# Performance work log

Measured on AMD Instinct MI355X. Metric: run time of the kernel, lower is better.

Reference implementation:

```python
import jax, jax.numpy as jnp
import numpy as np


def setup_inputs() -> dict:
    key = jax.random.key(0)
    ks = jax.random.split(key, 8)
    B, C, H, W = 4, 512, 64, 64
    C8 = C // 8
    return {
        "x": jax.random.normal(ks[0], (B, C, H, W), dtype=jnp.float32),
        "Wq": jax.random.normal(ks[1], (C8, C), dtype=jnp.float32) * 0.02,
        "bq": jax.random.normal(ks[2], (C8,), dtype=jnp.float32) * 0.02,
        "Wk": jax.random.normal(ks[3], (C8, C), dtype=jnp.float32) * 0.02,
        "bk": jax.random.normal(ks[4], (C8,), dtype=jnp.float32) * 0.02,
        "Wv": jax.random.normal(ks[5], (C, C), dtype=jnp.float32) * 0.02,
        "bv": jax.random.normal(ks[6], (C,), dtype=jnp.float32) * 0.02,
        "gamma": jax.random.normal(ks[7], (1,), dtype=jnp.float32),
    }


def reference(x, Wq, bq, Wk, bk, Wv, bv, gamma):
    B, C, H, W = x.shape
    N = H * W
    xf = x.reshape(B, C, N)  # 1x1 conv == per-position matmul over channels
    q = jnp.einsum('oc,bcn->bno', Wq, xf) + bq  # B, N, C//8  (proj_query^T)
    k = jnp.einsum('oc,bcn->bon', Wk, xf) + bk[None, :, None]  # B, C//8, N
    v = jnp.einsum('oc,bcn->bon', Wv, xf) + bv[None, :, None]  # B, C, N
    energy = jnp.einsum('bno,bom->bnm', q, k)  # B, N, N
    attention = jax.nn.softmax(energy, axis=-1)
    # out = bmm(proj_value, attention^T): out[:, :, n] = sum_m v[:, :, m] * att[n, m]
    out = jnp.einsum('bcm,bnm->bcn', v, attention).reshape(B, C, H, W)
    return gamma[0] * out + x
```

## Files before the change

kernel.cpp:

```cpp
#include <hip/hip_runtime.h>
#include <stdint.h>


typedef unsigned short u16;
typedef unsigned char u8;
typedef __attribute__((ext_vector_type(8))) short short8;
typedef __attribute__((ext_vector_type(4))) float f32x4;
typedef __attribute__((ext_vector_type(16))) float f32x16;
typedef __attribute__((ext_vector_type(4))) int i32x4;
typedef __attribute__((ext_vector_type(8))) int i32x8;

#define ASYNC16(gp, lp)                                                        \
  __builtin_amdgcn_global_load_lds(                                            \
      (__attribute__((address_space(1))) void*)(void*)(gp),                    \
      (__attribute__((address_space(3))) void*)(lp), 16, 0, 0)

#define WAIT_VM0 0x0F70
#define WAIT_VM3 0x0F73
#define WAIT_LGKM0 0xC07F

#define EXP_SHIFT 5.0f
#define EXP_CAP 57000.0f

__device__ __forceinline__ u16 f2bf(float f) {
  uint32_t u = __float_as_uint(f);
  u += 0x7FFFu + ((u >> 16) & 1u);
  return (u16)(u >> 16);
}

__device__ __forceinline__ u8 f2fp8(float f) {
  f = fminf(fmaxf(f, -440.f), 440.f);
  int r = __builtin_amdgcn_cvt_pk_fp8_f32(f, f, 0, false);
  return (u8)(r & 0xFF);
}

__global__ __launch_bounds__(256) void k_transpose(const float* __restrict__ x,
                                                   u16* __restrict__ xT) {
  __shared__ float tile[32][33];
  const int b = blockIdx.z;
  const int nb = blockIdx.x * 32;
  const int cb = blockIdx.y * 32;
  const int t = threadIdx.x;
  {
    const int nl = t & 31, c0 = t >> 5;
    const float* xp = x + ((size_t)b * 512 + cb) * 4096 + nb;
#pragma unroll
    for (int i = 0; i < 4; ++i) {
      const int cl = c0 + i * 8;
      tile[cl][nl] = xp[(size_t)cl * 4096 + nl];
    }
  }
  __syncthreads();
  {
    const int cl = t & 31, n0 = t >> 5;
    u16* xtp = xT + ((size_t)b * 4096 + nb) * 512 + cb;
#pragma unroll
    for (int i = 0; i < 4; ++i) {
      const int nl = n0 + i * 8;
      xtp[(size_t)nl * 512 + cl] = f2bf(tile[cl][nl]);
    }
  }
}

__global__ __launch_bounds__(256) void k_wcast(const float* __restrict__ Wq,
                                               const float* __restrict__ Wk,
                                               const float* __restrict__ Wv,
                                               u16* __restrict__ wqk,
                                               u16* __restrict__ wv) {
  const int idx = blockIdx.x * 256 + threadIdx.x;
  if (idx < 128 * 512) {
    const int r = idx >> 9, c = idx & 511;
    const float f = (r < 64) ? Wq[r * 512 + c] : Wk[(r - 64) * 512 + c];
    wqk[idx] = f2bf(f);
  } else {
    const int j = idx - 128 * 512;
    if (j < 512 * 512) wv[j] = f2bf(Wv[j]);
  }
}

__device__ __forceinline__ void gemm_bt_tile(const u16* __restrict__ A,
                                             const u16* __restrict__ B,
                                             const int K, const int rowA0,
                                             const int colB0, u16* smem,
                                             f32x4 acc[4][4]) {
  const int t = threadIdx.x;
  const int lane = t & 63, wave = t >> 6;
  const int quad = lane >> 4, l15 = lane & 15;
  const int wr = wave >> 1, wc = wave & 1;
  u16* As = smem;
  u16* Bs = smem + 8192;
  const f32x4 zero = {0.f, 0.f, 0.f, 0.f};
#pragma unroll
  for (int i = 0; i < 4; ++i)
#pragma unroll
    for (int j = 0; j < 4; ++j) acc[i][j] = zero;

  const int srow = t >> 3;
  const int c8 = (lane & 7) ^ (lane >> 3);
  const u16* ga = A + (size_t)(rowA0 + srow) * K + c8 * 8;
  const u16* gb = B + (size_t)(colB0 + srow) * K + c8 * 8;
  char* la = (char*)As + wave * 1024;
  char* lb = (char*)Bs + wave * 1024;
  const size_t rK32 = (size_t)32 * K;

  const int sw0 = (quad) ^ (l15 & 7);
  const int sw1 = (4 + quad) ^ (l15 & 7);

  for (int k0 = 0; k0 < K; k0 += 64) {
    ASYNC16(ga + k0, la);
    ASYNC16(ga + k0 + rK32, la + 4096);
    ASYNC16(ga + k0 + 2 * rK32, la + 8192);
    ASYNC16(ga + k0 + 3 * rK32, la + 12288);
    ASYNC16(gb + k0, lb);
    ASYNC16(gb + k0 + rK32, lb + 4096);
    ASYNC16(gb + k0 + 2 * rK32, lb + 8192);
    ASYNC16(gb + k0 + 3 * rK32, lb + 12288);
    __syncthreads();
#pragma unroll
    for (int s = 0; s < 2; ++s) {
      const int sw = s ? sw1 : sw0;
      short8 a[4], b[4];
#pragma unroll
      for (int i = 0; i < 4; ++i)
        a[i] = *(const short8*)(As + (wr * 64 + i * 16 + l15) * 64 + sw * 8);
#pragma unroll
      for (int j = 0; j < 4; ++j)
        b[j] = *(const short8*)(Bs + (wc * 64 + j * 16 + l15) * 64 + sw * 8);
#pragma unroll
      for (int i = 0; i < 4; ++i)
#pragma unroll
        for (int j = 0; j < 4; ++j)
          acc[i][j] = __builtin_amdgcn_mfma_f32_16x16x32_bf16(a[i], b[j],
                                                              acc[i][j], 0, 0, 0);
    }
    __syncthreads();
  }
}

__global__ __launch_bounds__(256) void k_proj(const u16* __restrict__ xT,
                                              const u16* __restrict__ wqk,
                                              const u16* __restrict__ wv,
                                              const float* __restrict__ bq,
                                              const float* __restrict__ bk,
                                              const float* __restrict__ bv,
                                              u16* __restrict__ q,
                                              u16* __restrict__ kT,
                                              u8* __restrict__ v8) {
  __shared__ u16 smem[16384];
  const int b = blockIdx.z;
  const int by = blockIdx.y;
  const int t = threadIdx.x, lane = t & 63, wave = t >> 6;
  const int quad = lane >> 4, l15 = lane & 15;
  const int wr = wave >> 1, wc = wave & 1;
  f32x4 acc[4][4];

  if (by == 4) {
    const int rowA0 = blockIdx.x * 128;
    gemm_bt_tile(xT + (size_t)b * 4096 * 512, wqk, 512, rowA0, 0, smem, acc);
#pragma unroll
    for (int j = 0; j < 4; ++j) {
      const int col = wc * 64 + j * 16 + l15;
      const float bias = (col < 64) ? bq[col] : bk[col - 64];
#pragma unroll
      for (int i = 0; i < 4; ++i) {
#pragma unroll
        for (int r = 0; r < 4; ++r) {
          const int row = rowA0 + wr * 64 + i * 16 + quad * 4 + r;
          const float val = acc[i][j][r] + bias;
          if (col < 64)
            q[((size_t)b * 4096 + row) * 64 + col] = f2bf(val);
          else
            kT[((size_t)b * 4096 + row) * 64 + (col - 64)] = f2bf(val);
        }
      }
    }
  } else {
    const int rowA0 = by * 128;
    const int colB0 = blockIdx.x * 128;
    gemm_bt_tile(wv, xT + (size_t)b * 4096 * 512, 512, rowA0, colB0, smem, acc);
#pragma unroll
    for (int i = 0; i < 4; ++i) {
#pragma unroll
      for (int r = 0; r < 4; ++r) {
        const int row = rowA0 + wr * 64 + i * 16 + quad * 4 + r;
        const float bias = bv[row];
#pragma unroll
        for (int j = 0; j < 4; ++j) {
          const int col = colB0 + wc * 64 + j * 16 + l15;
          v8[((size_t)b * 512 + row) * 4096 + col] = f2fp8(acc[i][j][r] + bias);
        }
      }
    }
  }
}

__global__ __launch_bounds__(1024, 4) void k_fused(
    const u16* __restrict__ q, const u16* __restrict__ kT,
    const u8* __restrict__ v8, const float* __restrict__ x,
    const float* __restrict__ gamma, float* __restrict__ out) {
  __shared__ u16 k_lds[2][128 * 64];
  __shared__ u8 v_lds[2][2][256 * 64];
  __shared__ u8 P_lds[2][128 * 64];
  __shared__ float lsum_lds[8][128];

  const int t = threadIdx.x;
  const int l = t & 63, w = t >> 6;
  const int quad = l >> 4, l15 = l & 15;
  const int l31 = l & 31, h = l >> 5;

  const int n0 = blockIdx.x * 128;
  const int c0 = blockIdx.y * 256;
  const int b = blockIdx.z;

  const u16* qg = q + ((size_t)b * 4096 + n0) * 64;
  const u16* kg = kT + (size_t)b * 4096 * 64;
  const u8* vg = v8 + ((size_t)b * 512 + c0) * 4096;

  const int kr = t >> 3, kc = t & 7;
  const u16* qsg = qg + kr * 64 + (kc ^ (kr & 7)) * 8;
  const u16* ksg = kg + kr * 64 + (kc ^ (kr & 7)) * 8;
  const int vr = t >> 2, va = t & 3;
  const u8* vsg = vg + (size_t)vr * 4096 + (va ^ ((vr >> 1) & 3)) * 16;

#define STAGE_F(bi, m0)                                                        \
  do {                                                                         \
    ASYNC16(ksg + (size_t)(m0) * 64, (char*)k_lds[bi] + w * 1024);             \
    ASYNC16(vsg + (m0), (char*)v_lds[bi][0] + w * 1024);                       \
    ASYNC16(vsg + (m0) + 64, (char*)v_lds[bi][1] + w * 1024);                  \
  } while (0)

  ASYNC16(qsg, (char*)P_lds[0] + w * 1024);
  STAGE_F(0, 0);
  __builtin_amdgcn_s_waitcnt(WAIT_VM3);
  __builtin_amdgcn_s_barrier();
  asm volatile("" ::: "memory");
  const int ms = w >> 1, nh = w & 1;
  const int sw0 = quad ^ (l15 & 7);
  const int sw1 = (4 + quad) ^ (l15 & 7);
  short8 af[4][2];
#pragma unroll
  for (int s = 0; s < 4; ++s) {
    const u16* qrow = (const u16*)P_lds[0] + (nh * 64 + s * 16 + l15) * 64;
    af[s][0] = *(const short8*)(qrow + sw0 * 8);
    af[s][1] = *(const short8*)(qrow + sw1 * 8);
  }
  asm volatile("" ::: "memory");
  __builtin_amdgcn_s_waitcnt(WAIT_LGKM0);
  __builtin_amdgcn_s_barrier();
  asm volatile("" ::: "memory");

  const int wrp = w >> 2, wcp = w & 3;
  int rowA[2], sA1[2], sA2[2];
#pragma unroll
  for (int i = 0; i < 2; ++i) {
    rowA[i] = wrp * 64 + i * 32 + l31;
    const int fa = (rowA[i] >> 1) & 3;
    sA1[i] = (2 * h) ^ fa;
    sA2[i] = (2 * h + 1) ^ fa;
  }
  const int rowB = wcp * 32 + l31;
  const int fbB = (rowB >> 1) & 3;
  const int sB1 = (2 * h) ^ fbB;
  const int sB2 = (2 * h + 1) ^ fbB;

  const int fbW = (l15 >> 1) & 3;
  u8* Pwbase = P_lds[ms >> 2] + (nh * 64 + l15) * 64 +
               (((ms & 3) ^ fbW) * 16) + quad * 4;

  const int krow_off = (ms * 16 + l15) * 64;

  f32x16 acc[2];
#pragma unroll
  for (int i = 0; i < 2; ++i)
#pragma unroll
    for (int r = 0; r < 16; ++r) acc[i][r] = 0.f;

  float lsums[4] = {0.f, 0.f, 0.f, 0.f};
  const f32x4 zero = {0.f, 0.f, 0.f, 0.f};

  for (int it = 0; it < 32; ++it) {
    __builtin_amdgcn_s_waitcnt(WAIT_VM0);
    asm volatile("" ::: "memory");
    __builtin_amdgcn_s_barrier();
    asm volatile("" ::: "memory");
    const int cur = it & 1;
    if (it + 1 < 32) STAGE_F(cur ^ 1, (it + 1) * 128);

    const u16* kb = k_lds[cur];
    const short8 kf0 = *(const short8*)(kb + krow_off + sw0 * 8);
    const short8 kf1 = *(const short8*)(kb + krow_off + sw1 * 8);
    f32x4 eacc[4];
#pragma unroll
    for (int s = 0; s < 4; ++s) eacc[s] = zero;
    __builtin_amdgcn_s_setprio(1);
#pragma unroll
    for (int s = 0; s < 4; ++s)
      eacc[s] = __builtin_amdgcn_mfma_f32_16x16x32_bf16(kf0, af[s][0],
                                                        eacc[s], 0, 0, 0);
#pragma unroll
    for (int s = 0; s < 4; ++s)
      eacc[s] = __builtin_amdgcn_mfma_f32_16x16x32_bf16(kf1, af[s][1],
                                                        eacc[s], 0, 0, 0);
    __builtin_amdgcn_s_setprio(0);

#pragma unroll
    for (int s = 0; s < 4; ++s) {
      const float e0 = fminf(__expf(eacc[s][0] - EXP_SHIFT), EXP_CAP);
      const float e1 = fminf(__expf(eacc[s][1] - EXP_SHIFT), EXP_CAP);
      const float e2 = fminf(__expf(eacc[s][2] - EXP_SHIFT), EXP_CAP);
      const float e3 = fminf(__expf(eacc[s][3] - EXP_SHIFT), EXP_CAP);
      lsums[s] += (e0 + e1) + (e2 + e3);
      int pk = __builtin_amdgcn_cvt_pk_bf8_f32(e0, e1, 0, false);
      pk = __builtin_amdgcn_cvt_pk_bf8_f32(e2, e3, pk, true);
      *(int*)(Pwbase + s * 1024) = pk;
    }
    asm volatile("" ::: "memory");
    __builtin_amdgcn_s_waitcnt(WAIT_LGKM0);
    __builtin_amdgcn_s_barrier();
    asm volatile("" ::: "memory");

#pragma unroll
    for (int ks = 0; ks < 2; ++ks) {
      const u8* Vb = v_lds[cur][ks];
      const u8* Pb = P_lds[ks];
      i32x8 bb;
      {
        const u8* pb = Pb + rowB * 64;
        const i32x4 blo = *(const i32x4*)(pb + sB1 * 16);
        const i32x4 bhi = *(const i32x4*)(pb + sB2 * 16);
        bb[0] = blo[0]; bb[1] = blo[1]; bb[2] = blo[2]; bb[3] = blo[3];
        bb[4] = bhi[0]; bb[5] = bhi[1]; bb[6] = bhi[2]; bb[7] = bhi[3];
      }
      __builtin_amdgcn_s_setprio(1);
#pragma unroll
      for (int i = 0; i < 2; ++i) {
        const u8* pa = Vb + rowA[i] * 64;
        const i32x4 lo = *(const i32x4*)(pa + sA1[i] * 16);
        const i32x4 hi = *(const i32x4*)(pa + sA2[i] * 16);
        i32x8 a;
        a[0] = lo[0]; a[1] = lo[1]; a[2] = lo[2]; a[3] = lo[3];
        a[4] = hi[0]; a[5] = hi[1]; a[6] = hi[2]; a[7] = hi[3];
        acc[i] = __builtin_amdgcn_mfma_scale_f32_32x32x64_f8f6f4(
            a, bb, acc[i], 0 , 1 , 0, 0x7F, 0, 0x7F);
      }
      __builtin_amdgcn_s_setprio(0);
    }
    asm volatile("" ::: "memory");
  }
#undef STAGE_F

#pragma unroll
  for (int s = 0; s < 4; ++s) {
    lsums[s] += __shfl_xor(lsums[s], 16);
    lsums[s] += __shfl_xor(lsums[s], 32);
  }
  if (l < 16) {
#pragma unroll
    for (int s = 0; s < 4; ++s)
      lsum_lds[ms][nh * 64 + s * 16 + l] = lsums[s];
  }
  asm volatile("" ::: "memory");
  __builtin_amdgcn_s_waitcnt(WAIT_LGKM0);
  __builtin_amdgcn_s_barrier();
  asm volatile("" ::: "memory");

  const float g = gamma[0];
  const int col = n0 + wcp * 32 + l31;
  const int nc = wcp * 32 + l31;
  float den = 0.f;
#pragma unroll
  for (int m = 0; m < 8; ++m) den += lsum_lds[m][nc];
  const float gil = g / den;
#pragma unroll
  for (int i = 0; i < 2; ++i) {
#pragma unroll
    for (int r = 0; r < 16; ++r) {
      const int rloc = (r & 3) + 8 * (r >> 2) + 4 * h;
      const int row = c0 + wrp * 64 + i * 32 + rloc;
      const size_t idx = ((size_t)b * 512 + row) * 4096 + col;
      out[idx] = gil * acc[i][r] + x[idx];
    }
  }
}

extern "C" void kernel_launch(void* const* d_in, const int* in_sizes, int n_in,
                              void* d_out, int out_size, void* d_ws,
                              size_t ws_size, hipStream_t stream) {
  const float* x = (const float*)d_in[0];
  const float* Wq = (const float*)d_in[1];
  const float* bq = (const float*)d_in[2];
  const float* Wk = (const float*)d_in[3];
  const float* bk = (const float*)d_in[4];
  const float* Wv = (const float*)d_in[5];
  const float* bv = (const float*)d_in[6];
  const float* gamma = (const float*)d_in[7];
  float* out = (float*)d_out;

  char* ws = (char*)d_ws;
  u16* xT = (u16*)(ws);
  u16* wqk = (u16*)(ws + 16777216);
  u16* wv = (u16*)(ws + 16908288);
  u16* qb = (u16*)(ws + 17432576);
  u16* ktb = (u16*)(ws + 19529728);
  u8* v8 = (u8*)(ws + 21626880);

  k_transpose<<<dim3(128, 16, 4), 256, 0, stream>>>(x, xT);
  k_wcast<<<dim3(1280), 256, 0, stream>>>(Wq, Wk, Wv, wqk, wv);
  k_proj<<<dim3(32, 5, 4), 256, 0, stream>>>(xT, wqk, wv, bq, bk, bv,
                                             qb, ktb, v8);
  k_fused<<<dim3(32, 2, 4), 1024, 0, stream>>>(qb, ktb, v8, x, gamma, out);
}
```

Baseline: 197.1 us.

## Retile fused attention to full channels per block with V loaded straight to registers

Each block of the fused attention kernel now covers 64 query positions and all 512 channels instead of 128 positions and 256 channels. This removes the duplicated energy/softmax computation across the two channel halves. V tiles are now read directly from global memory into registers rather than staged through LDS, which shrinks LDS use. Blocks are mapped with an XCD-aware index so each batch's blocks share an XCD's L2. In exchange, V global loads sit on the critical path, guarded only by a vmcnt wait, and each block does less energy work per V byte.

Measured after the change: 274.4 us. +39.2%, slower.

```diff
diff --git a/kernel.cpp b/kernel.cpp
--- a/kernel.cpp
+++ b/kernel.cpp
@@ -16,7 +16,7 @@
       (__attribute__((address_space(3))) void*)(lp), 16, 0, 0)
 
 #define WAIT_VM0 0x0F70
-#define WAIT_VM3 0x0F73
+#define WAIT_VM1 0x0F71
 #define WAIT_LGKM0 0xC07F
 
 #define EXP_SHIFT 5.0f
@@ -199,48 +199,42 @@
     const u8* __restrict__ v8, const float* __restrict__ x,
     const float* __restrict__ gamma, float* __restrict__ out) {
   __shared__ u16 k_lds[2][128 * 64];
-  __shared__ u8 v_lds[2][2][256 * 64];
-  __shared__ u8 P_lds[2][128 * 64];
-  __shared__ float lsum_lds[8][128];
+  __shared__ u8 P_lds[2][64 * 64];
+  __shared__ float lsum_lds[8][64];
 
   const int t = threadIdx.x;
   const int l = t & 63, w = t >> 6;
   const int quad = l >> 4, l15 = l & 15;
   const int l31 = l & 31, h = l >> 5;
 
-  const int n0 = blockIdx.x * 128;
-  const int c0 = blockIdx.y * 256;
-  const int b = blockIdx.z;
+  const int bid = blockIdx.x;
+  const int xcd = bid & 7;
+  const int slot = bid >> 3;
+  const int b = xcd >> 1;
+  const int n_idx = (xcd & 1) * 32 + slot;
+  const int n0 = n_idx * 64;
 
   const u16* qg = q + ((size_t)b * 4096 + n0) * 64;
   const u16* kg = kT + (size_t)b * 4096 * 64;
-  const u8* vg = v8 + ((size_t)b * 512 + c0) * 4096;
+  const u8* vg = v8 + (size_t)b * 512 * 4096;
 
   const int kr = t >> 3, kc = t & 7;
+  const u16* ksg = kg + kr * 64 + (kc ^ (kr & 7)) * 8;
   const u16* qsg = qg + kr * 64 + (kc ^ (kr & 7)) * 8;
-  const u16* ksg = kg + kr * 64 + (kc ^ (kr & 7)) * 8;
-  const int vr = t >> 2, va = t & 3;
-  const u8* vsg = vg + (size_t)vr * 4096 + (va ^ ((vr >> 1) & 3)) * 16;
-
-#define STAGE_F(bi, m0)                                                        \
-  do {                                                                         \
-    ASYNC16(ksg + (size_t)(m0) * 64, (char*)k_lds[bi] + w * 1024);             \
-    ASYNC16(vsg + (m0), (char*)v_lds[bi][0] + w * 1024);                       \
-    ASYNC16(vsg + (m0) + 64, (char*)v_lds[bi][1] + w * 1024);                  \
-  } while (0)
-
-  ASYNC16(qsg, (char*)P_lds[0] + w * 1024);
-  STAGE_F(0, 0);
-  __builtin_amdgcn_s_waitcnt(WAIT_VM3);
+
+  ASYNC16(ksg, (char*)k_lds[0] + w * 1024);
+  if (w < 8) ASYNC16(qsg, (char*)P_lds[0] + w * 1024);
+  __builtin_amdgcn_s_waitcnt(WAIT_VM0);
   __builtin_amdgcn_s_barrier();
   asm volatile("" ::: "memory");
+
   const int ms = w >> 1, nh = w & 1;
   const int sw0 = quad ^ (l15 & 7);
   const int sw1 = (4 + quad) ^ (l15 & 7);
-  short8 af[4][2];
-#pragma unroll
-  for (int s = 0; s < 4; ++s) {
-    const u16* qrow = (const u16*)P_lds[0] + (nh * 64 + s * 16 + l15) * 64;
+  short8 af[2][2];
+#pragma unroll
+  for (int s = 0; s < 2; ++s) {
+    const u16* qrow = (const u16*)P_lds[0] + (nh * 32 + s * 16 + l15) * 64;
     af[s][0] = *(const short8*)(qrow + sw0 * 8);
     af[s][1] = *(const short8*)(qrow + sw1 * 8);
   }
@@ -249,22 +243,18 @@
   __builtin_amdgcn_s_barrier();
   asm volatile("" ::: "memory");
 
-  const int wrp = w >> 2, wcp = w & 3;
-  int rowA[2], sA1[2], sA2[2];
-#pragma unroll
-  for (int i = 0; i < 2; ++i) {
-    rowA[i] = wrp * 64 + i * 32 + l31;
-    const int fa = (rowA[i] >> 1) & 3;
-    sA1[i] = (2 * h) ^ fa;
-    sA2[i] = (2 * h + 1) ^ fa;
-  }
+  const int wrp = w >> 1, wcp = w & 1;
   const int rowB = wcp * 32 + l31;
   const int fbB = (rowB >> 1) & 3;
   const int sB1 = (2 * h) ^ fbB;
   const int sB2 = (2 * h + 1) ^ fbB;
+  const u8* vp[2];
+#pragma unroll
+  for (int i = 0; i < 2; ++i)
+    vp[i] = vg + (size_t)(wrp * 64 + i * 32 + l31) * 4096 + h * 32;
 
   const int fbW = (l15 >> 1) & 3;
-  u8* Pwbase = P_lds[ms >> 2] + (nh * 64 + l15) * 64 +
+  u8* Pwbase = P_lds[ms >> 2] + (nh * 32 + l15) * 64 +
                (((ms & 3) ^ fbW) * 16) + quad * 4;
 
   const int krow_off = (ms * 16 + l15) * 64;
@@ -275,7 +265,7 @@
 #pragma unroll
     for (int r = 0; r < 16; ++r) acc[i][r] = 0.f;
 
-  float lsums[4] = {0.f, 0.f, 0.f, 0.f};
+  float lsums[2] = {0.f, 0.f};
   const f32x4 zero = {0.f, 0.f, 0.f, 0.f};
 
   for (int it = 0; it < 32; ++it) {
@@ -284,27 +274,39 @@
     __builtin_amdgcn_s_barrier();
     asm volatile("" ::: "memory");
     const int cur = it & 1;
-    if (it + 1 < 32) STAGE_F(cur ^ 1, (it + 1) * 128);
+
+    i32x4 vA[2][2][2];
+#pragma unroll
+    for (int i = 0; i < 2; ++i)
+#pragma unroll
+      for (int ks = 0; ks < 2; ++ks)
+#pragma unroll
+        for (int hf = 0; hf < 2; ++hf)
+          vA[i][ks][hf] = *(const i32x4*)(vp[i] + it * 128 + ks * 64 + hf * 16);
+
+    if (it + 1 < 32)
+      ASYNC16(ksg + (size_t)(it + 1) * 128 * 64,
+              (char*)k_lds[cur ^ 1] + w * 1024);
 
     const u16* kb = k_lds[cur];
     const short8 kf0 = *(const short8*)(kb + krow_off + sw0 * 8);
     const short8 kf1 = *(const short8*)(kb + krow_off + sw1 * 8);
-    f32x4 eacc[4];
-#pragma unroll
-    for (int s = 0; s < 4; ++s) eacc[s] = zero;
+    f32x4 eacc[2];
+#pragma unroll
+    for (int s = 0; s < 2; ++s) eacc[s] = zero;
     __builtin_amdgcn_s_setprio(1);
 #pragma unroll
-    for (int s = 0; s < 4; ++s)
+    for (int s = 0; s < 2; ++s)
       eacc[s] = __builtin_amdgcn_mfma_f32_16x16x32_bf16(kf0, af[s][0],
                                                         eacc[s], 0, 0, 0);
 #pragma unroll
-    for (int s = 0; s < 4; ++s)
+    for (int s = 0; s < 2; ++s)
       eacc[s] = __builtin_amdgcn_mfma_f32_16x16x32_bf16(kf1, af[s][1],
                                                         eacc[s], 0, 0, 0);
     __builtin_amdgcn_s_setprio(0);
 
 #pragma unroll
-    for (int s = 0; s < 4; ++s) {
+    for (int s = 0; s < 2; ++s) {
       const float e0 = fminf(__expf(eacc[s][0] - EXP_SHIFT), EXP_CAP);
       const float e1 = fminf(__expf(eacc[s][1] - EXP_SHIFT), EXP_CAP);
       const float e2 = fminf(__expf(eacc[s][2] - EXP_SHIFT), EXP_CAP);
@@ -319,27 +321,26 @@
     __builtin_amdgcn_s_barrier();
     asm volatile("" ::: "memory");
 
+    if (it < 31)
+      __builtin_amdgcn_s_waitcnt(WAIT_VM1);
+    else
+      __builtin_amdgcn_s_waitcnt(WAIT_VM0);
+
 #pragma unroll
     for (int ks = 0; ks < 2; ++ks) {
-      const u8* Vb = v_lds[cur][ks];
       const u8* Pb = P_lds[ks];
       i32x8 bb;
       {
         const u8* pb = Pb + rowB * 64;
         const i32x4 blo = *(const i32x4*)(pb + sB1 * 16);
         const i32x4 bhi = *(const i32x4*)(pb + sB2 * 16);
-        bb[0] = blo[0]; bb[1] = blo[1]; bb[2] = blo[2]; bb[3] = blo[3];
-        bb[4] = bhi[0]; bb[5] = bhi[1]; bb[6] = bhi[2]; bb[7] = bhi[3];
+        bb = __builtin_shufflevector(blo, bhi, 0, 1, 2, 3, 4, 5, 6, 7);
       }
       __builtin_amdgcn_s_setprio(1);
 #pragma unroll
       for (int i = 0; i < 2; ++i) {
-        const u8* pa = Vb + rowA[i] * 64;
-        const i32x4 lo = *(const i32x4*)(pa + sA1[i] * 16);
-        const i32x4 hi = *(const i32x4*)(pa + sA2[i] * 16);
-        i32x8 a;
-        a[0] = lo[0]; a[1] = lo[1]; a[2] = lo[2]; a[3] = lo[3];
-        a[4] = hi[0]; a[5] = hi[1]; a[6] = hi[2]; a[7] = hi[3];
+        const i32x8 a = __builtin_shufflevector(vA[i][ks][0], vA[i][ks][1],
+                                                0, 1, 2, 3, 4, 5, 6, 7);
         acc[i] = __builtin_amdgcn_mfma_scale_f32_32x32x64_f8f6f4(
             a, bb, acc[i], 0 , 1 , 0, 0x7F, 0, 0x7F);
       }
@@ -347,17 +348,16 @@
     }
     asm volatile("" ::: "memory");
   }
-#undef STAGE_F
-
-#pragma unroll
-  for (int s = 0; s < 4; ++s) {
+
+#pragma unroll
+  for (int s = 0; s < 2; ++s) {
     lsums[s] += __shfl_xor(lsums[s], 16);
     lsums[s] += __shfl_xor(lsums[s], 32);
   }
   if (l < 16) {
 #pragma unroll
-    for (int s = 0; s < 4; ++s)
-      lsum_lds[ms][nh * 64 + s * 16 + l] = lsums[s];
+    for (int s = 0; s < 2; ++s)
+      lsum_lds[ms][nh * 32 + s * 16 + l] = lsums[s];
   }
   asm volatile("" ::: "memory");
   __builtin_amdgcn_s_waitcnt(WAIT_LGKM0);
@@ -376,7 +376,7 @@
 #pragma unroll
     for (int r = 0; r < 16; ++r) {
       const int rloc = (r & 3) + 8 * (r >> 2) + 4 * h;
-      const int row = c0 + wrp * 64 + i * 32 + rloc;
+      const int row = wrp * 64 + i * 32 + rloc;
       const size_t idx = ((size_t)b * 512 + row) * 4096 + col;
       out[idx] = gil * acc[i][r] + x[idx];
     }
@@ -408,5 +408,5 @@
   k_wcast<<<dim3(1280), 256, 0, stream>>>(Wq, Wk, Wv, wqk, wv);
   k_proj<<<dim3(32, 5, 4), 256, 0, stream>>>(xT, wqk, wv, bq, bk, bv,
                                              qb, ktb, v8);
-  k_fused<<<dim3(32, 2, 4), 1024, 0, stream>>>(qb, ktb, v8, x, gamma, out);
-}
+  k_fused<<<dim3(256), 1024, 0, stream>>>(qb, ktb, v8, x, gamma, out);
+}
```
